# Optimization experiments

Hardware: AMD Instinct MI355X
Metric: run time of the kernel (lower is better)

## Reference

```python
import jax, jax.numpy as jnp
import numpy as np

# ---- constants from the source module ----
N_SAMPLES = 2 ** 15          # exp.n_samples
N_FRAMES = 128
N_HARMONICS = 8
N_EVENTS = 8
FILT_SIZE = 16               # freq_domain_filter_size
N_NOTES = 128                # len(scale)
NYQ = 22050.0 / 2.0          # samplerate nyquist
MIN_F0 = 40.0 / NYQ
F0_SPAN = (3000.0 / NYQ) - MIN_F0
MIN_RES = 0.5
RES_SPAN = 1.0 - MIN_RES
B_EVENTS = 128               # batch(16) * n_events(8)

# packed layout (build_param_slices order):
SL_F0 = slice(0, N_NOTES)                       # 0:128
SL_AMP = slice(N_NOTES + N_FRAMES, N_NOTES + 2 * N_FRAMES)   # 256:384
SL_HAMP = slice(N_NOTES + 2 * N_FRAMES, N_NOTES + 2 * N_FRAMES + N_HARMONICS)  # 384:392
SL_HDEC = slice(N_NOTES + 2 * N_FRAMES + N_HARMONICS, N_NOTES + 2 * N_FRAMES + 2 * N_HARMONICS)  # 392:400
SL_FENV = slice(N_NOTES + 2 * N_FRAMES + 2 * N_HARMONICS, N_NOTES + 2 * N_FRAMES + 2 * N_HARMONICS + FILT_SIZE)  # 400:416


def interp_linear(x, out_size):
    """F.interpolate(..., mode='linear', align_corners=False) on last dim of [B,C,L]."""
    L = x.shape[-1]
    scale = L / out_size
    coords = (jnp.arange(out_size, dtype=x.dtype) + 0.5) * scale - 0.5
    coords = jnp.clip(coords, 0.0, L - 1)
    i0 = jnp.floor(coords).astype(jnp.int32)
    i1 = jnp.minimum(i0 + 1, L - 1)
    w = coords - i0.astype(x.dtype)
    return x[..., i0] * (1.0 - w) + x[..., i1] * w


def setup_inputs() -> dict:
    key = jax.random.key(0)
    k1, k2 = jax.random.split(key)
    packed = jax.random.uniform(k1, (B_EVENTS, N_NOTES + 2 * N_FRAMES + 2 * N_HARMONICS + FILT_SIZE), dtype=jnp.float32)
    # musical-scale center frequencies, normalized by nyquist (geometric 20..3000 Hz)
    hz = 20.0 * (3000.0 / 20.0) ** (np.arange(N_NOTES) / (N_NOTES - 1))
    frequencies = jnp.asarray(hz / NYQ, dtype=jnp.float32)
    global_amp = jnp.full((1,), 5000.0, dtype=jnp.float32)
    osc_amp = jnp.full((1,), 50.0, dtype=jnp.float32)
    noise = jax.random.uniform(k2, (B_EVENTS, 1, N_SAMPLES), dtype=jnp.float32, minval=-1.0, maxval=1.0)
    return {"packed": packed, "frequencies": frequencies, "global_amp": global_amp,
            "osc_amp": osc_amp, "noise": noise}


def reference(packed, frequencies, global_amp, osc_amp, noise):
    B = packed.shape[0]
    # ---- f0 (discrete): softmax over notes, expectation, squared, repeated per frame ----
    f0_scalar = jax.nn.softmax(packed[:, SL_F0], axis=-1) @ frequencies          # [B]
    f0 = (f0_scalar ** 2)[:, None, None] * jnp.ones((1, 1, N_FRAMES), packed.dtype)  # [B,1,F]
    f0 = f0 * NYQ
    f0 = MIN_F0 + f0 * F0_SPAN
    # (the torch line `f0 + f0 + f0_fine` has no assignment -> no effect; f0_fine unused)

    # ---- oscillator bank ----
    harm_factors = jnp.arange(1, N_HARMONICS + 1, dtype=packed.dtype)
    osc = f0 * harm_factors[None, :, None]                      # [B,H,F]
    radians = osc / NYQ * jnp.pi
    radians = jnp.where(radians >= jnp.pi, 0.0, radians)
    radians = interp_linear(radians, N_SAMPLES)                  # [B,H,S]
    osc_bank = jnp.sin(jnp.cumsum(radians, axis=-1)) * osc_amp   # [B,H,S]

    # ---- per-harmonic amplitude recurrence (scan over frames) ----
    harm_decay = MIN_RES + packed[:, SL_HDEC] * RES_SPAN         # [B,H]
    harm_amp = packed[:, SL_HAMP]                                # [B,H]
    amp = packed[:, SL_AMP][:, None, :] * 2.0 - 1.0              # [B,1,F]

    def step(current, amp_i):                                    # current [B,H], amp_i [B,1]
        cur = jnp.maximum(current + amp_i * harm_amp, 0.0)       # clamp(0, inf)
        return cur * harm_decay, cur

    amp_frames = jnp.moveaxis(amp[:, 0, :], 1, 0)[:, :, None]    # [F,B,1]
    _, res = jax.lax.scan(step, jnp.zeros((B, N_HARMONICS), packed.dtype), amp_frames)
    res = jnp.moveaxis(res, 0, 2)                                # [B,H,F]
    res_full = interp_linear(res, N_SAMPLES)                     # [B,H,S]

    # ---- FFT-filtered noise ----
    amp_full = interp_linear(amp, N_SAMPLES)                     # [B,1,S]
    nf = packed[:, SL_FENV][:, None, :]                          # [B,1,16]
    nf = interp_linear(nf, N_SAMPLES // 2)
    nf = jnp.pad(nf, ((0, 0), (0, 0), (0, 1)))                   # [B,1,S//2+1]
    noise_scaled = noise * global_amp
    spec = jnp.fft.rfft(noise_scaled, axis=-1, norm='ortho')
    filt = spec * nf
    noise_out = jnp.fft.irfft(filt, n=N_SAMPLES, axis=-1, norm='ortho')
    noise_out = noise_out * jnp.where(amp_full >= 0, amp_full, 0.2 * amp_full)  # leaky_relu(0.2)

    # ---- combine ----
    x = res_full * osc_bank                                      # [B,H,S]
    x = noise_out / N_HARMONICS + x                              # broadcast [B,1,S]
    x = x.reshape(-1, N_EVENTS, N_HARMONICS, N_SAMPLES)
    x = jnp.sum(x, axis=(1, 2)).reshape(-1, 1, N_SAMPLES)        # [batch,1,S]
    return x
```

## Files before the change

kernel.cpp:

```cpp
#include <hip/hip_runtime.h>
#include <math.h>

#define PCK_STRIDE 416
#define N_SAMPLES  32768
#define FFT_M      16384
#define HN         8192
#define B_EVENTS   128
#define N_GROUPS   16
#define NT         1024
#define PI_F 3.14159265358979323846f
#define RT2H 0.70710678118654752f

#define MAP(i) ((i) + (((i) >> 5) << 2))
#define LDS_H  9216

__device__ inline float filt_at(const float* __restrict__ f, int k) {
    if (k >= FFT_M) return 0.0f;
    float c = ((float)k + 0.5f) * (1.0f / 1024.0f) - 0.5f;
    c = fminf(fmaxf(c, 0.0f), 15.0f);
    int i0 = (int)floorf(c);
    int i1 = min(i0 + 1, 15);
    float w = c - (float)i0;
    return f[i0] * (1.0f - w) + f[i1] * w;
}

template<int L>
__device__ inline void r4_dif_stage(float2* z, int tid) {
    constexpr int q = L >> 2;
    constexpr float ang = -6.28318530717958647692f / (float)L;
    #pragma unroll 1
    for (int s = 0; s < (HN / 4) / NT; ++s) {
        int m = tid + s * NT;
        int t = m & (q - 1);
        int i0 = ((m & ~(q - 1)) << 2) | t;
        int ia = MAP(i0), ib = MAP(i0 + q), ic = MAP(i0 + 2 * q), id = MAP(i0 + 3 * q);
        float2 A = z[ia], B = z[ib], C = z[ic], D = z[id];
        float s1, c1; __sincosf(ang * (float)t, &s1, &c1);
        float c2 = c1 * c1 - s1 * s1, s2 = 2.0f * c1 * s1;
        float c3 = c2 * c1 - s2 * s1, s3 = c2 * s1 + s2 * c1;
        float s0r = A.x + C.x, s0i = A.y + C.y;
        float t1r = B.x + D.x, t1i = B.y + D.y;
        float d0r = A.x - C.x, d0i = A.y - C.y;
        float d1r = B.x - D.x, d1i = B.y - D.y;
        z[ia] = make_float2(s0r + t1r, s0i + t1i);
        float er = s0r - t1r, ei = s0i - t1i;
        z[ib] = make_float2(er * c2 - ei * s2, er * s2 + ei * c2);
        float fr = d0r + d1i, fi = d0i - d1r;
        z[ic] = make_float2(fr * c1 - fi * s1, fr * s1 + fi * c1);
        float gr = d0r - d1i, gi = d0i + d1r;
        z[id] = make_float2(gr * c3 - gi * s3, gr * s3 + gi * c3);
    }
    __syncthreads();
}

template<int L>
__device__ inline void r4_dit_stage(float2* z, int tid) {
    constexpr int q = L >> 2;
    constexpr float ang = 6.28318530717958647692f / (float)L;
    #pragma unroll 1
    for (int s = 0; s < (HN / 4) / NT; ++s) {
        int m = tid + s * NT;
        int t = m & (q - 1);
        int i0 = ((m & ~(q - 1)) << 2) | t;
        int ia = MAP(i0), ib = MAP(i0 + q), ic = MAP(i0 + 2 * q), id = MAP(i0 + 3 * q);
        float2 A = z[ia], B = z[ib], C = z[ic], D = z[id];
        float s1, c1; __sincosf(ang * (float)t, &s1, &c1);
        float c2 = c1 * c1 - s1 * s1, s2 = 2.0f * c1 * s1;
        float tbr = B.x * c2 - B.y * s2, tbi = B.x * s2 + B.y * c2;
        float tdr = D.x * c2 - D.y * s2, tdi = D.x * s2 + D.y * c2;
        float B0r = A.x + tbr, B0i = A.y + tbi;
        float B1r = A.x - tbr, B1i = A.y - tbi;
        float B2r = C.x + tdr, B2i = C.y + tdi;
        float B3r = C.x - tdr, B3i = C.y - tdi;
        float t0r = B2r * c1 - B2i * s1, t0i = B2r * s1 + B2i * c1;
        float t1r = -B3r * s1 - B3i * c1, t1i = B3r * c1 - B3i * s1;
        z[ia] = make_float2(B0r + t0r, B0i + t0i);
        z[ib] = make_float2(B1r + t1r, B1i + t1i);
        z[ic] = make_float2(B0r - t0r, B0i - t0i);
        z[id] = make_float2(B1r - t1r, B1i - t1i);
    }
    __syncthreads();
}

__global__ __launch_bounds__(NT)
void fft_half_kernel(
    const float* __restrict__ noise, const float* __restrict__ packed,
    const float* __restrict__ gamp, float2* __restrict__ hd,
    const float* __restrict__ freqs, float* __restrict__ rW, float* __restrict__ res)
{
    extern __shared__ float smem[];
    float2* z = (float2*)smem;
    float* filt = smem + 2 * LDS_H;
    const int half = blockIdx.x;
    const int b = blockIdx.y;
    const int tid = threadIdx.x;
    const float g = gamp[0];

    const float2* nz = (const float2*)(noise + (size_t)b * N_SAMPLES);
    if (half == 0) {
        #pragma unroll 1
        for (int s = 0; s < HN / NT; ++s) {
            int j = tid + s * NT;
            float2 v0 = nz[j];
            float2 v1 = nz[j + HN];
            z[MAP(j)] = make_float2((v0.x + v1.x) * g, (v0.y + v1.y) * g);
        }
    } else {
        #pragma unroll 1
        for (int s = 0; s < HN / NT; ++s) {
            int j = tid + s * NT;
            float2 v0 = nz[j];
            float2 v1 = nz[j + HN];
            float dr = (v0.x - v1.x) * g, di = (v0.y - v1.y) * g;
            float s1, c1; __sincosf((-PI_F / 8192.0f) * (float)j, &s1, &c1);
            z[MAP(j)] = make_float2(dr * c1 - di * s1, dr * s1 + di * c1);
        }
    }
    if (tid >= 64 && tid < 80) filt[tid - 64] = packed[b * PCK_STRIDE + 400 + (tid - 64)];

    if (half == 0 && tid < 64) {
        const float* row = packed + b * PCK_STRIDE;
        float n0 = row[tid], n1 = row[tid + 64];
        float fq0 = freqs[tid], fq1 = freqs[tid + 64];
        float mx = fmaxf(n0, n1);
        #pragma unroll
        for (int off = 32; off >= 1; off >>= 1) mx = fmaxf(mx, __shfl_xor(mx, off));
        float e0 = __expf(n0 - mx), e1 = __expf(n1 - mx);
        float den = e0 + e1, num = e0 * fq0 + e1 * fq1;
        #pragma unroll
        for (int off = 32; off >= 1; off >>= 1) {
            den += __shfl_xor(den, off);
            num += __shfl_xor(num, off);
        }
        float ampA = row[256 + tid] * 2.0f - 1.0f;
        float ampB = row[320 + tid] * 2.0f - 1.0f;
        int h = tid & 7;
        float ha = row[384 + h];
        float hdcy = 0.5f + row[392 + h] * 0.5f;
        const float MIN_F0 = 40.0f / 11025.0f;
        const float F0_SPAN = 3000.0f / 11025.0f - 40.0f / 11025.0f;
        float f0s = num / den;
        float f0 = MIN_F0 + f0s * f0s * 11025.0f * F0_SPAN;
        float r = f0 * (float)(h + 1) * (PI_F / 11025.0f);
        if (r >= PI_F) r = 0.0f;
        if (tid < 8) rW[b * 8 + tid] = r;
        float cur = 0.0f;
        float* rr = res + (b * 8 + h) * 128;
        for (int f = 0; f < 64; ++f) {
            float av = __shfl(ampA, f);
            float c = fmaxf(cur + av * ha, 0.0f);
            if (tid < 8) rr[f] = c;
            cur = c * hdcy;
        }
        for (int f = 0; f < 64; ++f) {
            float av = __shfl(ampB, f);
            float c = fmaxf(cur + av * ha, 0.0f);
            if (tid < 8) rr[64 + f] = c;
            cur = c * hdcy;
        }
    }
    __syncthreads();

    r4_dif_stage<8192>(z, tid);
    r4_dif_stage<2048>(z, tid);
    r4_dif_stage<512>(z, tid);
    r4_dif_stage<128>(z, tid);
    r4_dif_stage<32>(z, tid);

    #pragma unroll 1
    for (int s = 0; s < (HN / 8) / NT; ++s) {
        int m = ((HN / 8) / NT) * tid + s;
        float* base = (float*)(z + MAP(8 * m));
        float4 f0 = *(const float4*)(base);
        float4 f1 = *(const float4*)(base + 4);
        float4 f2 = *(const float4*)(base + 8);
        float4 f3 = *(const float4*)(base + 12);
        float t0r = f0.x + f2.x, t0i = f0.y + f2.y;
        float u0r = f0.x - f2.x, u0i = f0.y - f2.y;
        float t1r = f0.z + f2.z, t1i = f0.w + f2.w;
        float d1r = f0.z - f2.z, d1i = f0.w - f2.w;
        float u1r = RT2H * (d1r + d1i), u1i = RT2H * (d1i - d1r);
        float t2r = f1.x + f3.x, t2i = f1.y + f3.y;
        float d2r = f1.x - f3.x, d2i = f1.y - f3.y;
        float u2r = d2i, u2i = -d2r;
        float t3r = f1.z + f3.z, t3i = f1.w + f3.w;
        float d3r = f1.z - f3.z, d3i = f1.w - f3.w;
        float u3r = RT2H * (d3i - d3r), u3i = -RT2H * (d3r + d3i);
        float A0r = t0r + t2r, A0i = t0i + t2i;
        float A2r = t0r - t2r, A2i = t0i - t2i;
        float A1r = t1r + t3r, A1i = t1i + t3i;
        float e3r = t1r - t3r, e3i = t1i - t3i;
        float A3r = e3i, A3i = -e3r;
        float B0r = u0r + u2r, B0i = u0i + u2i;
        float B2r = u0r - u2r, B2i = u0i - u2i;
        float B1r = u1r + u3r, B1i = u1i + u3i;
        float f3r = u1r - u3r, f3i = u1i - u3i;
        float B3r = f3i, B3i = -f3r;
        f0.x = A0r + A1r; f0.y = A0i + A1i; f0.z = A0r - A1r; f0.w = A0i - A1i;
        f1.x = A2r + A3r; f1.y = A2i + A3i; f1.z = A2r - A3r; f1.w = A2i - A3i;
        f2.x = B0r + B1r; f2.y = B0i + B1i; f2.z = B0r - B1r; f2.w = B0i - B1i;
        f3.x = B2r + B3r; f3.y = B2i + B3i; f3.z = B2r - B3r; f3.w = B2i - B3i;
        *(float4*)(base) = f0; *(float4*)(base + 4) = f1;
        *(float4*)(base + 8) = f2; *(float4*)(base + 12) = f3;
    }
    __syncthreads();

    const float invM = 1.0f / (float)FFT_M;
    #pragma unroll 1
    for (int s = 0; s < (HN / 2) / NT; ++s) {
        int p = (tid + s * NT) << 1;
        int jj = (half << 13) | p;
        if (jj == 0) {
            float2 z0 = z[MAP(0)];
            float y = 0.5f * filt_at(filt, 0) * (z0.x + z0.y) * invM;
            z[MAP(0)] = make_float2(y, y);
            float H = filt_at(filt, 8192) * invM;
            float2 z1 = z[MAP(1)];
            z[MAP(1)] = make_float2(z1.x * H, z1.y * H);
        } else {
            int k = (int)(__brev((unsigned)jj) >> 18);
            int kq = FFT_M - k;
            int pk = MAP(p);
            int pq = MAP((int)(__brev((unsigned)kq) >> 18) & (HN - 1));
            float2 zk = z[pk];
            float2 zq = z[pq];
            float Er = 0.5f * (zk.x + zq.x), Ei = 0.5f * (zk.y - zq.y);
            float Or = 0.5f * (zk.y + zq.y), Oi = 0.5f * (zq.x - zk.x);
            float th = (float)k * (PI_F / (float)FFT_M);
            float s1, c1; __sincosf(th, &s1, &c1);
            float ts = -s1;
            float tOr = c1 * Or - ts * Oi;
            float tOi = c1 * Oi + ts * Or;
            float Hk = filt_at(filt, k);
            float Hq = filt_at(filt, kq);
            float Ykr = Hk * (Er + tOr), Yki = Hk * (Ei + tOi);
            float Cr  = Hq * (Er - tOr), Ci  = Hq * (Ei - tOi);
            float Ar = 0.5f * (Ykr + Cr), Ai = 0.5f * (Yki + Ci);
            float Br = 0.5f * (Ykr - Cr), Bi = 0.5f * (Yki - Ci);
            z[pk] = make_float2((Ar + ts * Br - c1 * Bi) * invM,
                                (Ai + c1 * Br + ts * Bi) * invM);
            z[pq] = make_float2((Ar + c1 * Bi - ts * Br) * invM,
                                (-Ai + c1 * Br + ts * Bi) * invM);
        }
    }
    __syncthreads();

    #pragma unroll 1
    for (int s = 0; s < (HN / 8) / NT; ++s) {
        int m = ((HN / 8) / NT) * tid + s;
        float* base = (float*)(z + MAP(8 * m));
        float4 f0 = *(const float4*)(base);
        float4 f1 = *(const float4*)(base + 4);
        float4 f2 = *(const float4*)(base + 8);
        float4 f3 = *(const float4*)(base + 12);
        float A0r = f0.x + f0.z, A0i = f0.y + f0.w;
        float A1r = f0.x - f0.z, A1i = f0.y - f0.w;
        float A2r = f1.x + f1.z, A2i = f1.y + f1.w;
        float A3r = f1.x - f1.z, A3i = f1.y - f1.w;
        float B0r = f2.x + f2.z, B0i = f2.y + f2.w;
        float B1r = f2.x - f2.z, B1i = f2.y - f2.w;
        float B2r = f3.x + f3.z, B2i = f3.y + f3.w;
        float B3r = f3.x - f3.z, B3i = f3.y - f3.w;
        float t0r = A0r + A2r, t0i = A0i + A2i;
        float t2r = A0r - A2r, t2i = A0i - A2i;
        float w3r = -A3i, w3i = A3r;
        float t1r = A1r + w3r, t1i = A1i + w3i;
        float t3r = A1r - w3r, t3i = A1i - w3i;
        float u0r = B0r + B2r, u0i = B0i + B2i;
        float u2r = B0r - B2r, u2i = B0i - B2i;
        float x3r = -B3i, x3i = B3r;
        float u1r = B1r + x3r, u1i = B1i + x3i;
        float u3r = B1r - x3r, u3i = B1i - x3i;
        float w1r = RT2H * (u1r - u1i), w1i = RT2H * (u1r + u1i);
        float w2r = -u2i,               w2i = u2r;
        float w5r = RT2H * (-u3r - u3i), w5i = RT2H * (u3r - u3i);
        f0.x = t0r + u0r; f0.y = t0i + u0i;
        f0.z = t1r + w1r; f0.w = t1i + w1i;
        f1.x = t2r + w2r; f1.y = t2i + w2i;
        f1.z = t3r + w5r; f1.w = t3i + w5i;
        f2.x = t0r - u0r; f2.y = t0i - u0i;
        f2.z = t1r - w1r; f2.w = t1i - w1i;
        f3.x = t2r - w2r; f3.y = t2i - w2i;
        f3.z = t3r - w5r; f3.w = t3i - w5i;
        *(float4*)(base) = f0; *(float4*)(base + 4) = f1;
        *(float4*)(base + 8) = f2; *(float4*)(base + 12) = f3;
    }
    __syncthreads();

    r4_dit_stage<32>(z, tid);
    r4_dit_stage<128>(z, tid);
    r4_dit_stage<512>(z, tid);
    r4_dit_stage<2048>(z, tid);
    r4_dit_stage<8192>(z, tid);

    float2* dst = hd + (size_t)b * FFT_M + (half << 13);
    #pragma unroll 1
    for (int s = 0; s < HN / NT; ++s) {
        int j = tid + s * NT;
        dst[j] = z[MAP(j)];
    }
}

__global__ __launch_bounds__(256) void assemble_kernel(
    const float* __restrict__ packed, const float* __restrict__ rW,
    const float* __restrict__ res, const float2* __restrict__ hd,
    const float* __restrict__ oamp, float* __restrict__ out)
{
    const int g = blockIdx.y;
    const int chunk = blockIdx.x;
    const int tid = threadIdx.x;
    const int n0 = chunk * 512 + 2 * tid;
    const int fb = 2 * chunk - 1;

    __shared__ float s_res[8][8][4];
    __shared__ float s_ampf[8][4];
    __shared__ float s_r[8][8];
    {
        int e = tid >> 5, rem = tid & 31, h = rem >> 2, j = rem & 3;
        int f = min(max(fb + j, 0), 127);
        s_res[e][h][j] = res[((g * 8 + e) * 8 + h) * 128 + f];
    }
    if (tid < 32) {
        int e = tid >> 2, j = tid & 3;
        int f = min(max(fb + j, 0), 127);
        s_ampf[e][j] = packed[(g * 8 + e) * PCK_STRIDE + 256 + f] * 2.0f - 1.0f;
    } else if (tid < 96) {
        int u = tid - 32;
        s_r[u >> 3][u & 7] = rW[g * 64 + u];
    }
    __syncthreads();

    float c0 = fminf(fmaxf(((float)n0 + 0.5f) * (1.0f / 256.0f) - 0.5f, 0.0f), 127.0f);
    float c1v = fminf(fmaxf(((float)n0 + 1.5f) * (1.0f / 256.0f) - 0.5f, 0.0f), 127.0f);
    int i00 = (int)floorf(c0);  float w0 = c0 - (float)i00;  int ja = i00 - fb;
    int i01 = (int)floorf(c1v); float w1 = c1v - (float)i01; int jb = i01 - fb;
    float wm0 = 1.0f - w0, wm1 = 1.0f - w1;
    float osc50 = oamp[0];
    float pn0 = (float)(n0 + 1), pn1 = (float)(n0 + 2);

    const int jl = ((chunk & 31) << 8) | tid;
    const bool lo = (chunk < 32);
    float sx, cx; __sincosf((PI_F / 8192.0f) * (float)jl, &sx, &cx);

    float acc0 = 0.0f, acc1 = 0.0f;
    #pragma unroll
    for (int e = 0; e < 8; ++e) {
        int b = g * 8 + e;
        const float2* hb = hd + (size_t)b * FFT_M;
        float2 U = hb[jl];
        float2 X = hb[jl + HN];
        float wr2 = X.x * cx - X.y * sx;
        float wi2 = X.x * sx + X.y * cx;
        float nr = lo ? (U.x + wr2) : (U.x - wr2);
        float ni = lo ? (U.y + wi2) : (U.y - wi2);
        float av0 = s_ampf[e][ja] * wm0 + s_ampf[e][ja + 1] * w0;
        float av1 = s_ampf[e][jb] * wm1 + s_ampf[e][jb + 1] * w1;
        acc0 += nr * ((av0 >= 0.0f) ? av0 : 0.2f * av0);
        acc1 += ni * ((av1 >= 0.0f) ? av1 : 0.2f * av1);
        float r1 = s_r[e][0];
        float sn0, cn0; __sincosf(pn0 * r1, &sn0, &cn0);
        float sn1, cn1; __sincosf(pn1 * r1, &sn1, &cn1);
        float c20 = 2.0f * cn0, c21 = 2.0f * cn1;
        float sm0 = 0.0f, sh0 = sn0;
        float sm1 = 0.0f, sh1 = sn1;
        #pragma unroll
        for (int h = 0; h < 8; ++h) {
            float rs0 = s_res[e][h][ja] * wm0 + s_res[e][h][ja + 1] * w0;
            float rs1 = s_res[e][h][jb] * wm1 + s_res[e][h][jb + 1] * w1;
            bool nzr = (s_r[e][h] != 0.0f);
            acc0 += rs0 * osc50 * (nzr ? sh0 : 0.0f);
            acc1 += rs1 * osc50 * (nzr ? sh1 : 0.0f);
            float nx0 = c20 * sh0 - sm0; sm0 = sh0; sh0 = nx0;
            float nx1 = c21 * sh1 - sm1; sm1 = sh1; sh1 = nx1;
        }
    }
    *(float2*)(out + (size_t)g * N_SAMPLES + n0) = make_float2(acc0, acc1);
}

extern "C" void kernel_launch(void* const* d_in, const int* in_sizes, int n_in,
                              void* d_out, int out_size, void* d_ws, size_t ws_size,
                              hipStream_t stream) {
    const float* packed = (const float*)d_in[0];
    const float* freqs  = (const float*)d_in[1];
    const float* gamp   = (const float*)d_in[2];
    const float* oamp   = (const float*)d_in[3];
    const float* noise  = (const float*)d_in[4];
    float* out = (float*)d_out;

    float* ws = (float*)d_ws;
    float2* hd = (float2*)ws;
    float* res = ws + (size_t)B_EVENTS * N_SAMPLES;
    float* rW  = res + B_EVENTS * 8 * 128;

    fft_half_kernel<<<dim3(2, B_EVENTS), NT, (2 * LDS_H + 16) * sizeof(float), stream>>>(
        noise, packed, gamp, hd, freqs, rW, res);
    assemble_kernel<<<dim3(N_SAMPLES / 512, N_GROUPS), 256, 0, stream>>>(
        packed, rW, res, hd, oamp, out);
}
```

Before: 107.5 us.

## Fuse first radix-4 DIF stage into load and last DIT stage into store

The initial radix-4 DIF butterfly (span 8192) is merged into the global-memory load loop, which now reads four strided noise elements per thread and applies the half-split twiddle before the butterfly. Symmetrically, the final DIT stage is merged into the global store loop. This removes two full LDS read/write passes and two barriers per block. In exchange it adds more sincos/twiddle arithmetic and register pressure in the load/store loops.

```diff
diff --git a/kernel.cpp b/kernel.cpp
--- a/kernel.cpp
+++ b/kernel.cpp
@@ -97,24 +97,48 @@
     const float g = gamp[0];
 
     const float2* nz = (const float2*)(noise + (size_t)b * N_SAMPLES);
-    if (half == 0) {
-        #pragma unroll 1
-        for (int s = 0; s < HN / NT; ++s) {
-            int j = tid + s * NT;
-            float2 v0 = nz[j];
-            float2 v1 = nz[j + HN];
-            z[MAP(j)] = make_float2((v0.x + v1.x) * g, (v0.y + v1.y) * g);
-        }
-    } else {
-        #pragma unroll 1
-        for (int s = 0; s < HN / NT; ++s) {
-            int j = tid + s * NT;
-            float2 v0 = nz[j];
-            float2 v1 = nz[j + HN];
-            float dr = (v0.x - v1.x) * g, di = (v0.y - v1.y) * g;
-            float s1, c1; __sincosf((-PI_F / 8192.0f) * (float)j, &s1, &c1);
-            z[MAP(j)] = make_float2(dr * c1 - di * s1, dr * s1 + di * c1);
-        }
+    #pragma unroll 1
+    for (int s = 0; s < 2; ++s) {
+        int j = tid + s * NT;
+        float2 a0 = nz[j],        a1 = nz[j + 8192];
+        float2 b0 = nz[j + 2048], b1 = nz[j + 10240];
+        float2 c0 = nz[j + 4096], c1v = nz[j + 12288];
+        float2 d0 = nz[j + 6144], d1 = nz[j + 14336];
+        float Arr, Aii, Brr, Bii, Crr, Cii, Drr, Dii;
+        if (half == 0) {
+            Arr = (a0.x + a1.x) * g; Aii = (a0.y + a1.y) * g;
+            Brr = (b0.x + b1.x) * g; Bii = (b0.y + b1.y) * g;
+            Crr = (c0.x + c1v.x) * g; Cii = (c0.y + c1v.y) * g;
+            Drr = (d0.x + d1.x) * g; Dii = (d0.y + d1.y) * g;
+        } else {
+            float sw, cw; __sincosf((-PI_F / 8192.0f) * (float)j, &sw, &cw);
+            float cwB = RT2H * (cw + sw), swB = RT2H * (sw - cw);
+            float cwC = sw,               swC = -cw;
+            float cwD = RT2H * (sw - cw), swD = -RT2H * (cw + sw);
+            float dr, di;
+            dr = (a0.x - a1.x) * g; di = (a0.y - a1.y) * g;
+            Arr = dr * cw - di * sw;  Aii = dr * sw + di * cw;
+            dr = (b0.x - b1.x) * g; di = (b0.y - b1.y) * g;
+            Brr = dr * cwB - di * swB; Bii = dr * swB + di * cwB;
+            dr = (c0.x - c1v.x) * g; di = (c0.y - c1v.y) * g;
+            Crr = dr * cwC - di * swC; Cii = dr * swC + di * cwC;
+            dr = (d0.x - d1.x) * g; di = (d0.y - d1.y) * g;
+            Drr = dr * cwD - di * swD; Dii = dr * swD + di * cwD;
+        }
+        float s1, c1; __sincosf((-6.28318530717958647692f / 8192.0f) * (float)j, &s1, &c1);
+        float c2 = c1 * c1 - s1 * s1, s2 = 2.0f * c1 * s1;
+        float c3 = c2 * c1 - s2 * s1, s3 = c2 * s1 + s2 * c1;
+        float s0r = Arr + Crr, s0i = Aii + Cii;
+        float t1r = Brr + Drr, t1i = Bii + Dii;
+        float d0r = Arr - Crr, d0i = Aii - Cii;
+        float d1r = Brr - Drr, d1i = Bii - Dii;
+        z[MAP(j)] = make_float2(s0r + t1r, s0i + t1i);
+        float er = s0r - t1r, ei = s0i - t1i;
+        z[MAP(j + 2048)] = make_float2(er * c2 - ei * s2, er * s2 + ei * c2);
+        float fr = d0r + d1i, fi = d0i - d1r;
+        z[MAP(j + 4096)] = make_float2(fr * c1 - fi * s1, fr * s1 + fi * c1);
+        float gr = d0r - d1i, gi = d0i + d1r;
+        z[MAP(j + 6144)] = make_float2(gr * c3 - gi * s3, gr * s3 + gi * c3);
     }
     if (tid >= 64 && tid < 80) filt[tid - 64] = packed[b * PCK_STRIDE + 400 + (tid - 64)];
 
@@ -161,7 +185,6 @@
     }
     __syncthreads();
 
-    r4_dif_stage<8192>(z, tid);
     r4_dif_stage<2048>(z, tid);
     r4_dif_stage<512>(z, tid);
     r4_dif_stage<128>(z, tid);
@@ -291,13 +314,27 @@
     r4_dit_stage<128>(z, tid);
     r4_dit_stage<512>(z, tid);
     r4_dit_stage<2048>(z, tid);
-    r4_dit_stage<8192>(z, tid);
 
     float2* dst = hd + (size_t)b * FFT_M + (half << 13);
     #pragma unroll 1
-    for (int s = 0; s < HN / NT; ++s) {
-        int j = tid + s * NT;
-        dst[j] = z[MAP(j)];
+    for (int s = 0; s < 2; ++s) {
+        int m = tid + s * NT;
+        float2 A = z[MAP(m)], B = z[MAP(m + 2048)];
+        float2 C = z[MAP(m + 4096)], D = z[MAP(m + 6144)];
+        float s1, c1; __sincosf((6.28318530717958647692f / 8192.0f) * (float)m, &s1, &c1);
+        float c2 = c1 * c1 - s1 * s1, s2 = 2.0f * c1 * s1;
+        float tbr = B.x * c2 - B.y * s2, tbi = B.x * s2 + B.y * c2;
+        float tdr = D.x * c2 - D.y * s2, tdi = D.x * s2 + D.y * c2;
+        float B0r = A.x + tbr, B0i = A.y + tbi;
+        float B1r = A.x - tbr, B1i = A.y - tbi;
+        float B2r = C.x + tdr, B2i = C.y + tdi;
+        float B3r = C.x - tdr, B3i = C.y - tdi;
+        float t0r = B2r * c1 - B2i * s1, t0i = B2r * s1 + B2i * c1;
+        float t1r = -B3r * s1 - B3i * c1, t1i = B3r * c1 - B3i * s1;
+        dst[m]        = make_float2(B0r + t0r, B0i + t0i);
+        dst[m + 2048] = make_float2(B1r + t1r, B1i + t1i);
+        dst[m + 4096] = make_float2(B0r - t0r, B0i - t0i);
+        dst[m + 6144] = make_float2(B1r - t1r, B1i - t1i);
     }
 }
 
```

Result: no change. 106.0 us (-1.4%).
